# Kernel optimization log

Hardware: AMD Instinct MI355X
Metric: run time of the kernel (lower is better)

## Reference

```python
import jax, jax.numpy as jnp
import numpy as np


def setup_inputs() -> dict:
    key = jax.random.key(0)
    k1, k2 = jax.random.split(key)
    B, S_ENC, S_DEC, D = 8, 2048, 2048, 1024
    enc_outputs = jax.random.normal(k1, (B, S_ENC, D), dtype=jnp.float32)
    dec_outputs = jax.random.normal(k2, (B, S_DEC, D), dtype=jnp.float32)
    return {"enc_outputs": enc_outputs, "dec_outputs": dec_outputs}


def reference(enc_outputs, dec_outputs):
    # scores: [B, S_enc, S_dec] = enc @ dec^T (unscaled)
    a_t = jnp.einsum('bed,btd->bet', enc_outputs, dec_outputs)
    a_t = jax.nn.softmax(a_t, axis=-1)
    # context: [B, S_dec, D] = a_t^T @ enc
    c_t = jnp.einsum('bet,bed->btd', a_t, enc_outputs)
    return c_t
```

## Files before the change

### kernel.cpp

```cpp
#include <hip/hip_runtime.h>
#include <math.h>


typedef _Float16 half8 __attribute__((ext_vector_type(8)));
typedef _Float16 half4v __attribute__((ext_vector_type(4)));
typedef float floatx16 __attribute__((ext_vector_type(16)));

#define BM 128
#define BN 128
#define BK 64
#define LOG2E 1.44269504088896340736f

__device__ __forceinline__ void async_load16(const _Float16* g, void* l) {
  __builtin_amdgcn_global_load_lds(
      (const __attribute__((address_space(1))) void*)g,
      (__attribute__((address_space(3))) void*)l, 16, 0, 0);
}

template <typename OutT, bool TRANS, int RN>
__global__ __launch_bounds__(256, 4) void gemm_bt(
    const _Float16* __restrict__ A, const _Float16* __restrict__ Bt,
    OutT* __restrict__ C, float2* __restrict__ part, int K, long strideA,
    long strideB, long strideC, int ldA, int ldB, int ldC) {
  constexpr int CPR = BK / 8;
  constexpr int SK = BK / 16;
  __shared__ alignas(16) char smem[TRANS ? (128 * 136 * 2) : (2 * BM * BK * 2)];
  __shared__ float2 cred[TRANS ? 256 : 1];
  _Float16* lds_a = (_Float16*)smem;
  _Float16* lds_b = (_Float16*)(smem + BM * BK * 2);

  const int b = blockIdx.z;
  A += (long)b * strideA;
  Bt += (long)b * strideB;
  C += (long)b * strideC;

  const int id = blockIdx.y * gridDim.x + blockIdx.x;
  const int xcd = id & 7;
  const int l = id >> 3;
  const int m0 = ((xcd & 3) * 4 + l / RN) * BM;
  const int n0 = ((xcd >> 2) * RN + l % RN) * BN;

  const int tid = threadIdx.x;
  const int lane = tid & 63;
  const int wave = tid >> 6;
  const int l31 = lane & 31;
  const int kh = lane >> 5;
  const int wm = (wave >> 1) * 64;
  const int wn = (wave & 1) * 64;

  floatx16 acc[2][2] = {};

  for (int k0 = 0; k0 < K; k0 += BK) {
#pragma unroll
    for (int c = 0; c < 4; ++c) {
      const int off = c * 4096 + wave * 1024 + lane * 16;
      const int row = off >> 7;
      const int ke = (((off >> 4) & (CPR - 1)) ^ (row & (CPR - 1))) * 8;
      async_load16(A + (long)(m0 + row) * ldA + k0 + ke, (char*)lds_a + off);
      async_load16(Bt + (long)(n0 + row) * ldB + k0 + ke, (char*)lds_b + off);
    }
    __syncthreads();

    half8 af[2][SK], bf[2][SK];
#pragma unroll
    for (int i = 0; i < 2; ++i) {
      const int ra = wm + i * 32 + l31;
      const int rb = wn + i * 32 + l31;
#pragma unroll
      for (int s = 0; s < SK; ++s) {
        const int ck = s * 2 + kh;
        af[i][s] = *(const half8*)((const char*)lds_a + ra * (BK * 2) +
                                   ((ck ^ (ra & (CPR - 1))) << 4));
        bf[i][s] = *(const half8*)((const char*)lds_b + rb * (BK * 2) +
                                   ((ck ^ (rb & (CPR - 1))) << 4));
      }
    }
#pragma unroll
    for (int s = 0; s < SK; ++s)
#pragma unroll
      for (int i = 0; i < 2; ++i)
#pragma unroll
        for (int j = 0; j < 2; ++j)
          acc[i][j] = __builtin_amdgcn_mfma_f32_32x32x16_f16(
              af[i][s], bf[j][s], acc[i][j], 0, 0, 0);
    __syncthreads();
  }

  if constexpr (TRANS) {
    _Float16(*TT)[136] = (_Float16(*)[136])smem;
#pragma unroll
    for (int i = 0; i < 2; ++i)
#pragma unroll
      for (int j = 0; j < 2; ++j) {
        const int tl = wn + j * 32 + l31;
#pragma unroll
        for (int g = 0; g < 4; ++g) {
          half4v h;
#pragma unroll
          for (int rr = 0; rr < 4; ++rr) h[rr] = (_Float16)acc[i][j][g * 4 + rr];
          *(half4v*)&TT[tl][wm + i * 32 + 4 * kh + g * 8] = h;
        }
      }
    __syncthreads();
#pragma unroll
    for (int p = 0; p < 8; ++p) {
      const int idx = p * 256 + tid;
      const int tl = idx >> 4;
      const int ck = idx & 15;
      *(half8*)((_Float16*)C + (long)(n0 + tl) * ldC + m0 + ck * 8) =
          *(const half8*)&TT[tl][ck * 8];
    }
    {
      const int e_l = tid & 127;
      const int th = tid >> 7;
      float m = -1e30f, s = 0.f;
#pragma unroll 8
      for (int t = th * 64; t < th * 64 + 64; ++t) {
        const float x = (float)TT[t][e_l];
        const float m2 = fmaxf(m, x);
        s = s * __expf(m - m2) + __expf(x - m2);
        m = m2;
      }
      cred[tid] = make_float2(m, s);
      __syncthreads();
      if (tid < 128) {
        const float2 a = cred[tid];
        const float2 o = cred[tid + 128];
        const float m2 = fmaxf(a.x, o.x);
        const float ss = a.y * __expf(a.x - m2) + o.y * __expf(o.x - m2);
        part[((long)(n0 >> 7) * 8 + b) * 2048 + m0 + tid] =
            make_float2(m2, ss);
      }
    }
  } else {
#pragma unroll
    for (int i = 0; i < 2; ++i) {
      const int r_base = m0 + wm + i * 32 + 4 * kh;
#pragma unroll
      for (int j = 0; j < 2; ++j) {
        const int col = n0 + wn + j * 32 + l31;
#pragma unroll
        for (int g = 0; g < 4; ++g)
#pragma unroll
          for (int rr = 0; rr < 4; ++rr)
            C[(long)(r_base + g * 8 + rr) * ldC + col] =
                (OutT)acc[i][j][g * 4 + rr];
      }
    }
  }
}

__global__ __launch_bounds__(256) void conv_enc(const float* __restrict__ E,
                                                _Float16* __restrict__ Eh,
                                                _Float16* __restrict__ EhT,
                                                int Se, int D) {
  __shared__ _Float16 T[64][72];
  const int b = blockIdx.z;
  const int d0 = blockIdx.x * 64;
  const int e0 = blockIdx.y * 64;
  const float* Eb = E + (size_t)b * Se * D;
  _Float16* Ehb = Eh + (size_t)b * Se * D;
  _Float16* EhTb = EhT + (size_t)b * D * Se;
  const int tid = threadIdx.x;
  const int tx = tid & 15;
  const int ty = tid >> 4;

  half4v h[4];
#pragma unroll
  for (int r = 0; r < 4; ++r) {
    const int e = e0 + ty * 4 + r;
    float4 v = *(const float4*)(Eb + (size_t)e * D + d0 + tx * 4);
    h[r][0] = (_Float16)v.x; h[r][1] = (_Float16)v.y;
    h[r][2] = (_Float16)v.z; h[r][3] = (_Float16)v.w;
    *(half4v*)(Ehb + (size_t)e * D + d0 + tx * 4) = h[r];
  }
#pragma unroll
  for (int c = 0; c < 4; ++c) {
    half4v w;
#pragma unroll
    for (int r = 0; r < 4; ++r) w[r] = h[r][c];
    *(half4v*)&T[tx * 4 + c][ty * 4] = w;
  }
  __syncthreads();
#pragma unroll
  for (int p = 0; p < 2; ++p) {
    const int idx = tid + p * 256;
    const int row = idx >> 3;
    const int ck = idx & 7;
    *(half8*)(EhTb + (size_t)(d0 + row) * Se + e0 + ck * 8) =
        *(const half8*)&T[row][ck * 8];
  }
}

__global__ __launch_bounds__(256) void conv_dec(const float* __restrict__ X,
                                                _Float16* __restrict__ Y) {
  const size_t i = ((size_t)blockIdx.x * 256 + threadIdx.x) * 8;
  float4 a = *(const float4*)(X + i);
  float4 b = *(const float4*)(X + i + 4);
  half8 h;
  h[0] = (_Float16)a.x; h[1] = (_Float16)a.y;
  h[2] = (_Float16)a.z; h[3] = (_Float16)a.w;
  h[4] = (_Float16)b.x; h[5] = (_Float16)b.y;
  h[6] = (_Float16)b.z; h[7] = (_Float16)b.w;
  *(half8*)(Y + i) = h;
}

__global__ __launch_bounds__(256) void stats_combine(
    const float2* __restrict__ part, float* __restrict__ q) {
  const int idx = blockIdx.x * 256 + threadIdx.x;
  const int b = idx >> 11;
  const int e = idx & 2047;
  float2 a = part[(long)b * 2048 + e];
#pragma unroll
  for (int tb = 1; tb < 16; ++tb) {
    const float2 o = part[((long)tb * 8 + b) * 2048 + e];
    const float m2 = fmaxf(a.x, o.x);
    a.y = a.y * __expf(a.x - m2) + o.y * __expf(o.x - m2);
    a.x = m2;
  }
  q[idx] = a.x * LOG2E + log2f(a.y);
}

__global__ __launch_bounds__(256) void norm_stream(
    const _Float16* __restrict__ ST, const float* __restrict__ q,
    _Float16* __restrict__ P) {
  const int b = blockIdx.y;
  const int t0 = blockIdx.x * 4;
  const int e = threadIdx.x * 8;
  float4 q0 = *(const float4*)(q + (size_t)b * 2048 + e);
  float4 q1 = *(const float4*)(q + (size_t)b * 2048 + e + 4);
  const float qf[8] = {q0.x, q0.y, q0.z, q0.w, q1.x, q1.y, q1.z, q1.w};
  const size_t base = ((size_t)b * 2048 + t0) * 2048 + e;
#pragma unroll
  for (int r = 0; r < 4; ++r) {
    half8 v = *(const half8*)(ST + base + (size_t)r * 2048);
    half8 o;
#pragma unroll
    for (int j = 0; j < 8; ++j)
      o[j] = (_Float16)exp2f((float)v[j] * LOG2E - qf[j]);
    *(half8*)(P + base + (size_t)r * 2048) = o;
  }
}

extern "C" void kernel_launch(void* const* d_in, const int* in_sizes, int n_in,
                              void* d_out, int out_size, void* d_ws,
                              size_t ws_size, hipStream_t stream) {
  const float* enc = (const float*)d_in[0];
  const float* dec = (const float*)d_in[1];
  float* out = (float*)d_out;

  const int B = 8, SE = 2048, SD = 2048, D = 1024;
  char* ws = (char*)d_ws;
  _Float16* enc_h = (_Float16*)ws;
  _Float16* dec_h = (_Float16*)(ws + 33554432);
  _Float16* P = (_Float16*)ws;
  _Float16* enc_hT = (_Float16*)(ws + 67108864);
  _Float16* ST = (_Float16*)(ws + 100663296);
  float* q = (float*)(ws + 167772160);
  float2* part = (float2*)(ws + 167837696);

  conv_enc<<<dim3(D / 64, SE / 64, B), 256, 0, stream>>>(enc, enc_h, enc_hT,
                                                         SE, D);
  conv_dec<<<dim3((size_t)B * SD * D / 2048), 256, 0, stream>>>(dec, dec_h);
  gemm_bt<_Float16, true, 8><<<dim3(SD / BN, SE / BM, B), 256, 0, stream>>>(
      enc_h, dec_h, ST, part, D, (long)SE * D, (long)SD * D, (long)SE * SD, D,
      D, SE);
  stats_combine<<<dim3(64), 256, 0, stream>>>(part, q);
  norm_stream<<<dim3(512, B), 256, 0, stream>>>(ST, q, P);
  gemm_bt<float, false, 4><<<dim3(D / BN, SD / BM, B), 256, 0, stream>>>(
      P, enc_hT, out, nullptr, SE, (long)SD * SE, (long)D * SE, (long)SD * D,
      SE, SE, D);
}
```

Measured before the change: 351.7 us.

## Use 256x128 tiles for the second GEMM and fuse the conversion kernels

Adds a gemm_wide kernel with 256x128 output tiles (4x2 MFMA tiles per wave) for the P x enc GEMM, raising operand reuse per LDS load compared with the 128x128 tile. The enc and dec fp32-to-fp16 conversions are merged into one conv_all launch, and norm_stream now handles 16 rows per block instead of 4. The larger tile uses more LDS and registers, which caps occupancy at 2 blocks per CU and gives fewer blocks in the grid.

Result: no change. 351.2 us (-0.1%).

```diff
diff --git a/kernel.cpp b/kernel.cpp
--- a/kernel.cpp
+++ b/kernel.cpp
@@ -17,15 +17,15 @@
       (__attribute__((address_space(3))) void*)l, 16, 0, 0);
 }
 
-template <typename OutT, bool TRANS, int RN>
+template <int RN>
 __global__ __launch_bounds__(256, 4) void gemm_bt(
     const _Float16* __restrict__ A, const _Float16* __restrict__ Bt,
-    OutT* __restrict__ C, float2* __restrict__ part, int K, long strideA,
+    _Float16* __restrict__ C, float2* __restrict__ part, int K, long strideA,
     long strideB, long strideC, int ldA, int ldB, int ldC) {
   constexpr int CPR = BK / 8;
   constexpr int SK = BK / 16;
-  __shared__ alignas(16) char smem[TRANS ? (128 * 136 * 2) : (2 * BM * BK * 2)];
-  __shared__ float2 cred[TRANS ? 256 : 1];
+  __shared__ alignas(16) char smem[128 * 136 * 2];
+  __shared__ float2 cred[256];
   _Float16* lds_a = (_Float16*)smem;
   _Float16* lds_b = (_Float16*)(smem + BM * BK * 2);
 
@@ -86,123 +86,196 @@
     __syncthreads();
   }
 
-  if constexpr (TRANS) {
-    _Float16(*TT)[136] = (_Float16(*)[136])smem;
-#pragma unroll
-    for (int i = 0; i < 2; ++i)
+  _Float16(*TT)[136] = (_Float16(*)[136])smem;
+#pragma unroll
+  for (int i = 0; i < 2; ++i)
+#pragma unroll
+    for (int j = 0; j < 2; ++j) {
+      const int tl = wn + j * 32 + l31;
+#pragma unroll
+      for (int g = 0; g < 4; ++g) {
+        half4v h;
+#pragma unroll
+        for (int rr = 0; rr < 4; ++rr) h[rr] = (_Float16)acc[i][j][g * 4 + rr];
+        *(half4v*)&TT[tl][wm + i * 32 + 4 * kh + g * 8] = h;
+      }
+    }
+  __syncthreads();
+#pragma unroll
+  for (int p = 0; p < 8; ++p) {
+    const int idx = p * 256 + tid;
+    const int tl = idx >> 4;
+    const int ck = idx & 15;
+    *(half8*)(C + (long)(n0 + tl) * ldC + m0 + ck * 8) =
+        *(const half8*)&TT[tl][ck * 8];
+  }
+  {
+    const int e_l = tid & 127;
+    const int th = tid >> 7;
+    float m = -1e30f, s = 0.f;
+#pragma unroll 8
+    for (int t = th * 64; t < th * 64 + 64; ++t) {
+      const float x = (float)TT[t][e_l];
+      const float m2 = fmaxf(m, x);
+      s = s * __expf(m - m2) + __expf(x - m2);
+      m = m2;
+    }
+    cred[tid] = make_float2(m, s);
+    __syncthreads();
+    if (tid < 128) {
+      const float2 a = cred[tid];
+      const float2 o = cred[tid + 128];
+      const float m2 = fmaxf(a.x, o.x);
+      const float ss = a.y * __expf(a.x - m2) + o.y * __expf(o.x - m2);
+      part[((long)(n0 >> 7) * 8 + b) * 2048 + m0 + tid] = make_float2(m2, ss);
+    }
+  }
+}
+
+template <int RM, int RN>
+__global__ __launch_bounds__(256, 2) void gemm_wide(
+    const _Float16* __restrict__ A, const _Float16* __restrict__ Bt,
+    float* __restrict__ C, int K, long strideA, long strideB, long strideC,
+    int ldA, int ldB, int ldC) {
+  __shared__ alignas(16) _Float16 lds_a[256 * 64];
+  __shared__ alignas(16) _Float16 lds_b[128 * 64];
+  const int b = blockIdx.z;
+  A += (long)b * strideA;
+  Bt += (long)b * strideB;
+  C += (long)b * strideC;
+  const int id = blockIdx.y * gridDim.x + blockIdx.x;
+  const int xcd = id & 7;
+  const int l = id >> 3;
+  const int m0 = ((xcd & 3) * RM + l / RN) * 256;
+  const int n0 = ((xcd >> 2) * RN + l % RN) * 128;
+  const int tid = threadIdx.x;
+  const int lane = tid & 63;
+  const int wave = tid >> 6;
+  const int l31 = lane & 31;
+  const int kh = lane >> 5;
+  const int wm = (wave >> 1) * 128;
+  const int wn = (wave & 1) * 64;
+
+  floatx16 acc[4][2] = {};
+
+  for (int k0 = 0; k0 < K; k0 += 64) {
+#pragma unroll
+    for (int c = 0; c < 8; ++c) {
+      const int off = c * 4096 + wave * 1024 + lane * 16;
+      const int row = off >> 7;
+      const int ke = (((off >> 4) & 7) ^ (row & 7)) * 8;
+      async_load16(A + (long)(m0 + row) * ldA + k0 + ke, (char*)lds_a + off);
+    }
+#pragma unroll
+    for (int c = 0; c < 4; ++c) {
+      const int off = c * 4096 + wave * 1024 + lane * 16;
+      const int row = off >> 7;
+      const int ke = (((off >> 4) & 7) ^ (row & 7)) * 8;
+      async_load16(Bt + (long)(n0 + row) * ldB + k0 + ke, (char*)lds_b + off);
+    }
+    __syncthreads();
+#pragma unroll
+    for (int s = 0; s < 4; ++s) {
+      const int ck = s * 2 + kh;
+      half8 af[4], bf[2];
+#pragma unroll
+      for (int i = 0; i < 4; ++i) {
+        const int ra = wm + i * 32 + l31;
+        af[i] = *(const half8*)((const char*)lds_a + ra * 128 +
+                                ((ck ^ (ra & 7)) << 4));
+      }
 #pragma unroll
       for (int j = 0; j < 2; ++j) {
-        const int tl = wn + j * 32 + l31;
-#pragma unroll
-        for (int g = 0; g < 4; ++g) {
-          half4v h;
-#pragma unroll
-          for (int rr = 0; rr < 4; ++rr) h[rr] = (_Float16)acc[i][j][g * 4 + rr];
-          *(half4v*)&TT[tl][wm + i * 32 + 4 * kh + g * 8] = h;
-        }
+        const int rb = wn + j * 32 + l31;
+        bf[j] = *(const half8*)((const char*)lds_b + rb * 128 +
+                                ((ck ^ (rb & 7)) << 4));
       }
-    __syncthreads();
-#pragma unroll
-    for (int p = 0; p < 8; ++p) {
-      const int idx = p * 256 + tid;
-      const int tl = idx >> 4;
-      const int ck = idx & 15;
-      *(half8*)((_Float16*)C + (long)(n0 + tl) * ldC + m0 + ck * 8) =
-          *(const half8*)&TT[tl][ck * 8];
-    }
-    {
-      const int e_l = tid & 127;
-      const int th = tid >> 7;
-      float m = -1e30f, s = 0.f;
-#pragma unroll 8
-      for (int t = th * 64; t < th * 64 + 64; ++t) {
-        const float x = (float)TT[t][e_l];
-        const float m2 = fmaxf(m, x);
-        s = s * __expf(m - m2) + __expf(x - m2);
-        m = m2;
-      }
-      cred[tid] = make_float2(m, s);
-      __syncthreads();
-      if (tid < 128) {
-        const float2 a = cred[tid];
-        const float2 o = cred[tid + 128];
-        const float m2 = fmaxf(a.x, o.x);
-        const float ss = a.y * __expf(a.x - m2) + o.y * __expf(o.x - m2);
-        part[((long)(n0 >> 7) * 8 + b) * 2048 + m0 + tid] =
-            make_float2(m2, ss);
-      }
-    }
-  } else {
-#pragma unroll
-    for (int i = 0; i < 2; ++i) {
-      const int r_base = m0 + wm + i * 32 + 4 * kh;
-#pragma unroll
-      for (int j = 0; j < 2; ++j) {
-        const int col = n0 + wn + j * 32 + l31;
-#pragma unroll
-        for (int g = 0; g < 4; ++g)
-#pragma unroll
-          for (int rr = 0; rr < 4; ++rr)
-            C[(long)(r_base + g * 8 + rr) * ldC + col] =
-                (OutT)acc[i][j][g * 4 + rr];
-      }
-    }
-  }
-}
-
-__global__ __launch_bounds__(256) void conv_enc(const float* __restrict__ E,
+#pragma unroll
+      for (int i = 0; i < 4; ++i)
+#pragma unroll
+        for (int j = 0; j < 2; ++j)
+          acc[i][j] = __builtin_amdgcn_mfma_f32_32x32x16_f16(af[i], bf[j],
+                                                             acc[i][j], 0, 0, 0);
+    }
+    __syncthreads();
+  }
+
+#pragma unroll
+  for (int i = 0; i < 4; ++i) {
+    const int r_base = m0 + wm + i * 32 + 4 * kh;
+#pragma unroll
+    for (int j = 0; j < 2; ++j) {
+      const int col = n0 + wn + j * 32 + l31;
+#pragma unroll
+      for (int g = 0; g < 4; ++g)
+#pragma unroll
+        for (int rr = 0; rr < 4; ++rr)
+          C[(long)(r_base + g * 8 + rr) * ldC + col] = acc[i][j][g * 4 + rr];
+    }
+  }
+}
+
+__global__ __launch_bounds__(256) void conv_all(const float* __restrict__ E,
+                                                const float* __restrict__ Dc,
                                                 _Float16* __restrict__ Eh,
                                                 _Float16* __restrict__ EhT,
-                                                int Se, int D) {
-  __shared__ _Float16 T[64][72];
+                                                _Float16* __restrict__ Dh) {
   const int b = blockIdx.z;
-  const int d0 = blockIdx.x * 64;
-  const int e0 = blockIdx.y * 64;
-  const float* Eb = E + (size_t)b * Se * D;
-  _Float16* Ehb = Eh + (size_t)b * Se * D;
-  _Float16* EhTb = EhT + (size_t)b * D * Se;
   const int tid = threadIdx.x;
-  const int tx = tid & 15;
-  const int ty = tid >> 4;
-
-  half4v h[4];
-#pragma unroll
-  for (int r = 0; r < 4; ++r) {
-    const int e = e0 + ty * 4 + r;
-    float4 v = *(const float4*)(Eb + (size_t)e * D + d0 + tx * 4);
-    h[r][0] = (_Float16)v.x; h[r][1] = (_Float16)v.y;
-    h[r][2] = (_Float16)v.z; h[r][3] = (_Float16)v.w;
-    *(half4v*)(Ehb + (size_t)e * D + d0 + tx * 4) = h[r];
-  }
-#pragma unroll
-  for (int c = 0; c < 4; ++c) {
-    half4v w;
-#pragma unroll
-    for (int r = 0; r < 4; ++r) w[r] = h[r][c];
-    *(half4v*)&T[tx * 4 + c][ty * 4] = w;
-  }
-  __syncthreads();
-#pragma unroll
-  for (int p = 0; p < 2; ++p) {
-    const int idx = tid + p * 256;
-    const int row = idx >> 3;
-    const int ck = idx & 7;
-    *(half8*)(EhTb + (size_t)(d0 + row) * Se + e0 + ck * 8) =
-        *(const half8*)&T[row][ck * 8];
-  }
-}
-
-__global__ __launch_bounds__(256) void conv_dec(const float* __restrict__ X,
-                                                _Float16* __restrict__ Y) {
-  const size_t i = ((size_t)blockIdx.x * 256 + threadIdx.x) * 8;
-  float4 a = *(const float4*)(X + i);
-  float4 b = *(const float4*)(X + i + 4);
-  half8 h;
-  h[0] = (_Float16)a.x; h[1] = (_Float16)a.y;
-  h[2] = (_Float16)a.z; h[3] = (_Float16)a.w;
-  h[4] = (_Float16)b.x; h[5] = (_Float16)b.y;
-  h[6] = (_Float16)b.z; h[7] = (_Float16)b.w;
-  *(half8*)(Y + i) = h;
+  if (blockIdx.x < 16) {
+    __shared__ _Float16 T[64][72];
+    const int d0 = blockIdx.x * 64;
+    const int e0 = blockIdx.y * 64;
+    const float* Eb = E + (size_t)b * 2048 * 1024;
+    _Float16* Ehb = Eh + (size_t)b * 2048 * 1024;
+    _Float16* EhTb = EhT + (size_t)b * 1024 * 2048;
+    const int tx = tid & 15;
+    const int ty = tid >> 4;
+    half4v h[4];
+#pragma unroll
+    for (int r = 0; r < 4; ++r) {
+      const int e = e0 + ty * 4 + r;
+      float4 v = *(const float4*)(Eb + (size_t)e * 1024 + d0 + tx * 4);
+      h[r][0] = (_Float16)v.x; h[r][1] = (_Float16)v.y;
+      h[r][2] = (_Float16)v.z; h[r][3] = (_Float16)v.w;
+      *(half4v*)(Ehb + (size_t)e * 1024 + d0 + tx * 4) = h[r];
+    }
+#pragma unroll
+    for (int c = 0; c < 4; ++c) {
+      half4v w;
+#pragma unroll
+      for (int r = 0; r < 4; ++r) w[r] = h[r][c];
+      *(half4v*)&T[tx * 4 + c][ty * 4] = w;
+    }
+    __syncthreads();
+#pragma unroll
+    for (int p = 0; p < 2; ++p) {
+      const int idx = tid + p * 256;
+      const int row = idx >> 3;
+      const int ck = idx & 7;
+      *(half8*)(EhTb + (size_t)(d0 + row) * 2048 + e0 + ck * 8) =
+          *(const half8*)&T[row][ck * 8];
+    }
+  } else {
+    const int d0 = (blockIdx.x - 16) * 128;
+    const int t0 = blockIdx.y * 64;
+    const float* Db = Dc + (size_t)b * 2048 * 1024;
+    _Float16* Dhb = Dh + (size_t)b * 2048 * 1024;
+    const int tx = tid & 15;
+    const int ty = tid >> 4;
+#pragma unroll
+    for (int r = 0; r < 4; ++r) {
+      const size_t o = (size_t)(t0 + ty + r * 16) * 1024 + d0 + tx * 8;
+      float4 a = *(const float4*)(Db + o);
+      float4 c = *(const float4*)(Db + o + 4);
+      half8 h;
+      h[0] = (_Float16)a.x; h[1] = (_Float16)a.y;
+      h[2] = (_Float16)a.z; h[3] = (_Float16)a.w;
+      h[4] = (_Float16)c.x; h[5] = (_Float16)c.y;
+      h[6] = (_Float16)c.z; h[7] = (_Float16)c.w;
+      *(half8*)(Dhb + o) = h;
+    }
+  }
 }
 
 __global__ __launch_bounds__(256) void stats_combine(
@@ -225,14 +298,14 @@
     const _Float16* __restrict__ ST, const float* __restrict__ q,
     _Float16* __restrict__ P) {
   const int b = blockIdx.y;
-  const int t0 = blockIdx.x * 4;
+  const int t0 = blockIdx.x * 16;
   const int e = threadIdx.x * 8;
   float4 q0 = *(const float4*)(q + (size_t)b * 2048 + e);
   float4 q1 = *(const float4*)(q + (size_t)b * 2048 + e + 4);
   const float qf[8] = {q0.x, q0.y, q0.z, q0.w, q1.x, q1.y, q1.z, q1.w};
   const size_t base = ((size_t)b * 2048 + t0) * 2048 + e;
-#pragma unroll
-  for (int r = 0; r < 4; ++r) {
+#pragma unroll 4
+  for (int r = 0; r < 16; ++r) {
     half8 v = *(const half8*)(ST + base + (size_t)r * 2048);
     half8 o;
 #pragma unroll
@@ -259,15 +332,14 @@
   float* q = (float*)(ws + 167772160);
   float2* part = (float2*)(ws + 167837696);
 
-  conv_enc<<<dim3(D / 64, SE / 64, B), 256, 0, stream>>>(enc, enc_h, enc_hT,
-                                                         SE, D);
-  conv_dec<<<dim3((size_t)B * SD * D / 2048), 256, 0, stream>>>(dec, dec_h);
-  gemm_bt<_Float16, true, 8><<<dim3(SD / BN, SE / BM, B), 256, 0, stream>>>(
+  conv_all<<<dim3(24, 32, B), 256, 0, stream>>>(enc, dec, enc_h, enc_hT,
+                                                dec_h);
+  gemm_bt<8><<<dim3(SD / BN, SE / BM, B), 256, 0, stream>>>(
       enc_h, dec_h, ST, part, D, (long)SE * D, (long)SD * D, (long)SE * SD, D,
       D, SE);
   stats_combine<<<dim3(64), 256, 0, stream>>>(part, q);
-  norm_stream<<<dim3(512, B), 256, 0, stream>>>(ST, q, P);
-  gemm_bt<float, false, 4><<<dim3(D / BN, SD / BM, B), 256, 0, stream>>>(
-      P, enc_hT, out, nullptr, SE, (long)SD * SE, (long)D * SE, (long)SD * D,
-      SE, SE, D);
-}
+  norm_stream<<<dim3(128, B), 256, 0, stream>>>(ST, q, P);
+  gemm_wide<2, 4><<<dim3(8, 8, B), 256, 0, stream>>>(
+      P, enc_hT, out, SE, (long)SD * SE, (long)D * SE, (long)SD * D, SE, SE,
+      D);
+}
```
